# Optimization experiments

Hardware: AMD Instinct MI355X
Metric: run time of the kernel (lower is better)

## Reference

```python
import jax, jax.numpy as jnp
import numpy as np

W, L, K, N = 32, 64, 512, 64


def setup_inputs() -> dict:
    key = jax.random.key(0)
    k0, k1, k2, k3 = jax.random.split(key, 4)
    # 0/1 spin states stored as float, matching torch.randint(0, 2, ..., dtype=float32)
    states = jax.random.randint(k0, (W, L, K, N), 0, 2).astype(jnp.float32)
    Q = jax.random.normal(k1, (W, N, N), dtype=jnp.float32)
    # inverse temperatures, ascending (standard parallel-tempering ladder)
    beta = jnp.sort(jax.random.uniform(k2, (L,), minval=0.1, maxval=2.0, dtype=jnp.float32))
    # uniform draws replacing torch.rand_like(delta) in exchange()
    u = jax.random.uniform(k3, (W, L - 1, K), dtype=jnp.float32)
    return {"states": states, "Q": Q, "beta": beta, "u": u}


def reference(states, Q, beta, u):
    """Temperer.exchange(): energies then masked replica swap.

    Returns (energies (W,L,K) before exchange, new states (W,L,K,N)).
    """
    # energy: einsum('wlki,wij,wlkj->wlk') done as one GEMM + elementwise reduce
    sQ = jnp.einsum('wlki,wij->wlkj', states, Q)          # (W,L,K,N)
    energies = jnp.einsum('wlkj,wlkj->wlk', sQ, states)   # (W,L,K)

    dbeta = (beta[1:] - beta[:-1])[None, :, None]          # (1,L-1,1)
    delta = (energies[:, 1:] - energies[:, :-1]) * dbeta   # (W,L-1,K)
    mask = (u < jnp.exp(delta)).astype(states.dtype)[..., None]  # (W,L-1,K,1)

    left = states[:, :-1]
    right = states[:, 1:]
    # replicate torch's sequential overlapping slice assignments exactly
    new = states.at[:, :-1].set(mask * right + (1.0 - mask) * left)
    new = new.at[:, 1:].set(mask * left + (1.0 - mask) * right)
    return energies, new
```

## Files before the change

### kernel.cpp

```cpp
#include <hip/hip_runtime.h>
#include <math.h>

#define PW 32
#define PL 64
#define PK 512
#define PN 64

typedef int   v4i __attribute__((ext_vector_type(4)));
typedef float v4f __attribute__((ext_vector_type(4)));


constexpr int ITERS_PER_WAVE = 4;

__global__ __launch_bounds__(256) void energies_kernel(
    const float* __restrict__ states, const float* __restrict__ Q,
    float* __restrict__ e_out, double* __restrict__ e64,
    unsigned long long* __restrict__ pmask)
{
    __shared__ alignas(16) signed char Afrag[16 * 64 * 16];

    const int tid  = threadIdx.x;
    const int lane = tid & 63;
    const int wv   = tid >> 6;
    const int w    = blockIdx.x >> 6;
    const int blk  = blockIdx.x & 63;

    const float* Qw = Q + w * PN * PN;
    for (int e = tid; e < PN * PN; e += 256) {
        const int i = e >> 6, j = e & 63;
        long long R = llrint((double)Qw[e] * 268435456.0);
        const int h = i & 3, b = i >> 2;
        const int frag_lane = (h << 4) | (j & 15);
        const int jt = j >> 4;
#pragma unroll
        for (int k = 0; k < 4; ++k) {
            const signed char d = (signed char)(R & 0xFF);
            R = (R - d) >> 8;
            Afrag[((k * 4 + jt) * 64 + frag_lane) * 16 + b] = d;
        }
    }
    __syncthreads();

    const v4i* Af = (const v4i*)Afrag;

    const long vw_base = (long)w * (PL * PK)
                       + (long)(blk * 4 + wv) * (32 * ITERS_PER_WAVE);
    const int h   = lane >> 4;
    const int g16 = (lane & 3) * 16;
    const int itA = (lane & 15) >> 2;
    const int itO = (lane & 31) >> 2;

    for (int t = 0; t < ITERS_PER_WAVE; ++t) {
        const long vbase = vw_base + (long)t * 32;

        unsigned long long pmA = 0, pmB = 0, pmO = 0;
#pragma unroll
        for (int it = 0; it < 8; ++it) {
            const v4f f = ((const v4f*)(states + (vbase + it * 4) * PN))[lane];
            const unsigned long long m0 = __ballot(f.x != 0.0f);
            const unsigned long long m1 = __ballot(f.y != 0.0f);
            const unsigned long long m2 = __ballot(f.z != 0.0f);
            const unsigned long long m3 = __ballot(f.w != 0.0f);
            const unsigned long long cand =
                  ((m0 >> g16) & 0xFFFFull)
                | (((m1 >> g16) & 0xFFFFull) << 16)
                | (((m2 >> g16) & 0xFFFFull) << 32)
                | (((m3 >> g16) & 0xFFFFull) << 48);
            pmA = (it == itA)     ? cand : pmA;
            pmB = (it == itA + 4) ? cand : pmB;
            pmO = (it == itO)     ? cand : pmO;
        }
        if (lane < 32) pmask[vbase + lane] = pmO;

        const unsigned int bA = (unsigned int)(pmA >> (h * 16)) & 0xFFFFu;
        const unsigned int bB = (unsigned int)(pmB >> (h * 16)) & 0xFFFFu;
        v4i BA, BB;
#pragma unroll
        for (int q = 0; q < 4; ++q) {
            BA[q] = (int)((((bA >> (4 * q)) & 0xFu) * 0x00204081u) & 0x01010101u);
            BB[q] = (int)((((bB >> (4 * q)) & 0xFu) * 0x00204081u) & 0x01010101u);
        }

        unsigned int xA[4], xB[4];
#pragma unroll
        for (int r = 0; r < 4; ++r) {
            xA[r] = (unsigned int)(pmA >> (r * 16 + h)) & 0x1111u;
            xB[r] = (unsigned int)(pmB >> (r * 16 + h)) & 0x1111u;
        }

        long long accA = 0, accB = 0;
#pragma unroll
        for (int k = 0; k < 4; ++k) {
            v4i A0 = Af[(k * 4 + 0) * 64 + lane];
            v4i A1 = Af[(k * 4 + 1) * 64 + lane];
            v4i A2 = Af[(k * 4 + 2) * 64 + lane];
            v4i A3 = Af[(k * 4 + 3) * 64 + lane];
            v4i CA0 = {0,0,0,0}, CA1 = {0,0,0,0}, CA2 = {0,0,0,0}, CA3 = {0,0,0,0};
            v4i CB0 = {0,0,0,0}, CB1 = {0,0,0,0}, CB2 = {0,0,0,0}, CB3 = {0,0,0,0};
            asm("s_nop 1\n\t"
                "v_mfma_i32_16x16x64_i8 %0, %8, %12, %0\n\t"
                "v_mfma_i32_16x16x64_i8 %4, %8, %13, %4\n\t"
                "v_mfma_i32_16x16x64_i8 %1, %9, %12, %1\n\t"
                "v_mfma_i32_16x16x64_i8 %5, %9, %13, %5\n\t"
                "v_mfma_i32_16x16x64_i8 %2, %10, %12, %2\n\t"
                "v_mfma_i32_16x16x64_i8 %6, %10, %13, %6\n\t"
                "v_mfma_i32_16x16x64_i8 %3, %11, %12, %3\n\t"
                "v_mfma_i32_16x16x64_i8 %7, %11, %13, %7\n\t"
                "s_nop 7\n\t"
                "s_nop 7"
                : "+v"(CA0), "+v"(CA1), "+v"(CA2), "+v"(CA3),
                  "+v"(CB0), "+v"(CB1), "+v"(CB2), "+v"(CB3)
                : "v"(A0), "v"(A1), "v"(A2), "v"(A3), "v"(BA), "v"(BB));
            int akA = 0, akB = 0;
#pragma unroll
            for (int r = 0; r < 4; ++r) {
                akA += ((xA[r] >> 0)  & 1) * CA0[r];
                akA += ((xA[r] >> 4)  & 1) * CA1[r];
                akA += ((xA[r] >> 8)  & 1) * CA2[r];
                akA += ((xA[r] >> 12) & 1) * CA3[r];
                akB += ((xB[r] >> 0)  & 1) * CB0[r];
                akB += ((xB[r] >> 4)  & 1) * CB1[r];
                akB += ((xB[r] >> 8)  & 1) * CB2[r];
                akB += ((xB[r] >> 12) & 1) * CB3[r];
            }
            accA += (long long)akA << (8 * k);
            accB += (long long)akB << (8 * k);
        }

        accA += __shfl_xor(accA, 16, 64);
        accA += __shfl_xor(accA, 32, 64);
        accB += __shfl_xor(accB, 16, 64);
        accB += __shfl_xor(accB, 32, 64);

        if (lane < 16) {
            const double eA = (double)accA * 0x1p-28;
            const double eB = (double)accB * 0x1p-28;
            e64[vbase + lane]        = eA;
            e_out[vbase + lane]      = (float)eA;
            e64[vbase + 16 + lane]   = eB;
            e_out[vbase + 16 + lane] = (float)eB;
        }
    }
}

__global__ __launch_bounds__(256) void swap_kernel(
    const unsigned long long* __restrict__ pmask,
    const double* __restrict__ e64,
    const float* __restrict__ beta, const float* __restrict__ u,
    float* __restrict__ out)
{
    const long row0 = (long)blockIdx.x * 16;
    const int tid = threadIdx.x;
    const long row = row0 + (tid >> 4);
    const int e = tid & 15;
    const int w = (int)(row >> 15);
    const int l = (int)((row >> 9) & 63);
    const int k = (int)(row & 511);

    long src;
    if (l == 0) {
        const double db = (double)beta[1] - (double)beta[0];
        const double delta = (e64[row + PK] - e64[row]) * db;
        const float uv = u[(long)w * (PL - 1) * PK + k];
        src = row + (((double)uv < exp(delta)) ? PK : 0);
    } else {
        const double db = (double)beta[l] - (double)beta[l - 1];
        const double delta = (e64[row] - e64[row - PK]) * db;
        const float uv = u[((long)w * (PL - 1) + (l - 1)) * PK + k];
        src = row - (((double)uv < exp(delta)) ? PK : 0);
    }

    const unsigned long long pm = pmask[src];
    v4f f;
    f.x = ((pm >> e)        & 1) ? 1.0f : 0.0f;
    f.y = ((pm >> (16 + e)) & 1) ? 1.0f : 0.0f;
    f.z = ((pm >> (32 + e)) & 1) ? 1.0f : 0.0f;
    f.w = ((pm >> (48 + e)) & 1) ? 1.0f : 0.0f;
    ((v4f*)(out + row * PN))[e] = f;
}

extern "C" void kernel_launch(void* const* d_in, const int* in_sizes, int n_in,
                              void* d_out, int out_size, void* d_ws, size_t ws_size,
                              hipStream_t stream) {
    const float* states = (const float*)d_in[0];
    const float* Q      = (const float*)d_in[1];
    const float* beta   = (const float*)d_in[2];
    const float* u      = (const float*)d_in[3];

    float* e_out      = (float*)d_out;
    float* new_states = (float*)d_out + (long)PW * PL * PK;

    const long NV = (long)PW * PL * PK;
    double* e64 = (double*)d_ws;
    unsigned long long* pmask = (unsigned long long*)((char*)d_ws + 8 * NV);

    energies_kernel<<<2048, 256, 0, stream>>>(states, Q, e_out, e64, pmask);

    swap_kernel<<<65536, 256, 0, stream>>>(pmask, e64, beta, u, new_states);
}
```

Measured before the change: 513.5 us.

## Hoist Q fragments to registers, batch state loads, restructure swap kernel per-row decisions

Energies kernel now processes twice as many rows per wave with half the blocks, hoists all 16 Q fragments from LDS into registers once, and issues all eight state loads up front before the ballot packing to increase memory-level parallelism. Swap kernel computes one accept decision per row per thread (instead of 16 redundant threads per row), stages source offsets in shared memory, then writes 256 rows per block. This removes redundant exp/e64 loads in the swap and LDS reloads in the energy pass, at the cost of higher register pressure and fewer blocks.

```diff
diff --git a/kernel.cpp b/kernel.cpp
--- a/kernel.cpp
+++ b/kernel.cpp
@@ -10,9 +10,11 @@
 typedef float v4f __attribute__((ext_vector_type(4)));
 
 
-constexpr int ITERS_PER_WAVE = 4;
-
-__global__ __launch_bounds__(256) void energies_kernel(
+constexpr int ITERS_PER_WAVE = 8;
+
+#define DECLA(n) v4i A##n = Af[(n) * 64 + lane];
+
+__global__ __launch_bounds__(256, 3) void energies_kernel(
     const float* __restrict__ states, const float* __restrict__ Q,
     float* __restrict__ e_out, double* __restrict__ e64,
     unsigned long long* __restrict__ pmask)
@@ -22,8 +24,8 @@
     const int tid  = threadIdx.x;
     const int lane = tid & 63;
     const int wv   = tid >> 6;
-    const int w    = blockIdx.x >> 6;
-    const int blk  = blockIdx.x & 63;
+    const int w    = blockIdx.x >> 5;
+    const int blk  = blockIdx.x & 31;
 
     const float* Qw = Q + w * PN * PN;
     for (int e = tid; e < PN * PN; e += 256) {
@@ -43,6 +45,11 @@
 
     const v4i* Af = (const v4i*)Afrag;
 
+    DECLA(0)  DECLA(1)  DECLA(2)  DECLA(3)
+    DECLA(4)  DECLA(5)  DECLA(6)  DECLA(7)
+    DECLA(8)  DECLA(9)  DECLA(10) DECLA(11)
+    DECLA(12) DECLA(13) DECLA(14) DECLA(15)
+
     const long vw_base = (long)w * (PL * PK)
                        + (long)(blk * 4 + wv) * (32 * ITERS_PER_WAVE);
     const int h   = lane >> 4;
@@ -52,24 +59,36 @@
 
     for (int t = 0; t < ITERS_PER_WAVE; ++t) {
         const long vbase = vw_base + (long)t * 32;
+        const float* sp = states + vbase * PN;
+
+        v4f f0 = ((const v4f*)(sp          ))[lane];
+        v4f f1 = ((const v4f*)(sp +  4 * PN))[lane];
+        v4f f2 = ((const v4f*)(sp +  8 * PN))[lane];
+        v4f f3 = ((const v4f*)(sp + 12 * PN))[lane];
+        v4f f4 = ((const v4f*)(sp + 16 * PN))[lane];
+        v4f f5 = ((const v4f*)(sp + 20 * PN))[lane];
+        v4f f6 = ((const v4f*)(sp + 24 * PN))[lane];
+        v4f f7 = ((const v4f*)(sp + 28 * PN))[lane];
 
         unsigned long long pmA = 0, pmB = 0, pmO = 0;
-#pragma unroll
-        for (int it = 0; it < 8; ++it) {
-            const v4f f = ((const v4f*)(states + (vbase + it * 4) * PN))[lane];
-            const unsigned long long m0 = __ballot(f.x != 0.0f);
-            const unsigned long long m1 = __ballot(f.y != 0.0f);
-            const unsigned long long m2 = __ballot(f.z != 0.0f);
-            const unsigned long long m3 = __ballot(f.w != 0.0f);
-            const unsigned long long cand =
-                  ((m0 >> g16) & 0xFFFFull)
-                | (((m1 >> g16) & 0xFFFFull) << 16)
-                | (((m2 >> g16) & 0xFFFFull) << 32)
-                | (((m3 >> g16) & 0xFFFFull) << 48);
-            pmA = (it == itA)     ? cand : pmA;
-            pmB = (it == itA + 4) ? cand : pmB;
-            pmO = (it == itO)     ? cand : pmO;
-        }
+#define PACK_IT(it, ff)                                                    \
+        {                                                                  \
+            const unsigned long long m0 = __ballot(ff.x != 0.0f);          \
+            const unsigned long long m1 = __ballot(ff.y != 0.0f);          \
+            const unsigned long long m2 = __ballot(ff.z != 0.0f);          \
+            const unsigned long long m3 = __ballot(ff.w != 0.0f);          \
+            const unsigned long long cand =                                \
+                  ((m0 >> g16) & 0xFFFFull)                                \
+                | (((m1 >> g16) & 0xFFFFull) << 16)                        \
+                | (((m2 >> g16) & 0xFFFFull) << 32)                        \
+                | (((m3 >> g16) & 0xFFFFull) << 48);                       \
+            pmA = ((it) == itA)     ? cand : pmA;                          \
+            pmB = ((it) == itA + 4) ? cand : pmB;                          \
+            pmO = ((it) == itO)     ? cand : pmO;                          \
+        }
+        PACK_IT(0, f0) PACK_IT(1, f1) PACK_IT(2, f2) PACK_IT(3, f3)
+        PACK_IT(4, f4) PACK_IT(5, f5) PACK_IT(6, f6) PACK_IT(7, f7)
+#undef PACK_IT
         if (lane < 32) pmask[vbase + lane] = pmO;
 
         const unsigned int bA = (unsigned int)(pmA >> (h * 16)) & 0xFFFFu;
@@ -89,43 +108,44 @@
         }
 
         long long accA = 0, accB = 0;
-#pragma unroll
-        for (int k = 0; k < 4; ++k) {
-            v4i A0 = Af[(k * 4 + 0) * 64 + lane];
-            v4i A1 = Af[(k * 4 + 1) * 64 + lane];
-            v4i A2 = Af[(k * 4 + 2) * 64 + lane];
-            v4i A3 = Af[(k * 4 + 3) * 64 + lane];
-            v4i CA0 = {0,0,0,0}, CA1 = {0,0,0,0}, CA2 = {0,0,0,0}, CA3 = {0,0,0,0};
-            v4i CB0 = {0,0,0,0}, CB1 = {0,0,0,0}, CB2 = {0,0,0,0}, CB3 = {0,0,0,0};
-            asm("s_nop 1\n\t"
-                "v_mfma_i32_16x16x64_i8 %0, %8, %12, %0\n\t"
-                "v_mfma_i32_16x16x64_i8 %4, %8, %13, %4\n\t"
-                "v_mfma_i32_16x16x64_i8 %1, %9, %12, %1\n\t"
-                "v_mfma_i32_16x16x64_i8 %5, %9, %13, %5\n\t"
-                "v_mfma_i32_16x16x64_i8 %2, %10, %12, %2\n\t"
-                "v_mfma_i32_16x16x64_i8 %6, %10, %13, %6\n\t"
-                "v_mfma_i32_16x16x64_i8 %3, %11, %12, %3\n\t"
-                "v_mfma_i32_16x16x64_i8 %7, %11, %13, %7\n\t"
-                "s_nop 7\n\t"
-                "s_nop 7"
-                : "+v"(CA0), "+v"(CA1), "+v"(CA2), "+v"(CA3),
-                  "+v"(CB0), "+v"(CB1), "+v"(CB2), "+v"(CB3)
-                : "v"(A0), "v"(A1), "v"(A2), "v"(A3), "v"(BA), "v"(BB));
-            int akA = 0, akB = 0;
-#pragma unroll
-            for (int r = 0; r < 4; ++r) {
-                akA += ((xA[r] >> 0)  & 1) * CA0[r];
-                akA += ((xA[r] >> 4)  & 1) * CA1[r];
-                akA += ((xA[r] >> 8)  & 1) * CA2[r];
-                akA += ((xA[r] >> 12) & 1) * CA3[r];
-                akB += ((xB[r] >> 0)  & 1) * CB0[r];
-                akB += ((xB[r] >> 4)  & 1) * CB1[r];
-                akB += ((xB[r] >> 8)  & 1) * CB2[r];
-                akB += ((xB[r] >> 12) & 1) * CB3[r];
-            }
-            accA += (long long)akA << (8 * k);
-            accB += (long long)akB << (8 * k);
-        }
+#define DIGIT_K(k, a0, a1, a2, a3)                                          \
+        {                                                                   \
+            v4i CA0 = {0,0,0,0}, CA1 = {0,0,0,0}, CA2 = {0,0,0,0}, CA3 = {0,0,0,0}; \
+            v4i CB0 = {0,0,0,0}, CB1 = {0,0,0,0}, CB2 = {0,0,0,0}, CB3 = {0,0,0,0}; \
+            asm("s_nop 1\n\t"                                               \
+                "v_mfma_i32_16x16x64_i8 %0, %8, %12, %0\n\t"                \
+                "v_mfma_i32_16x16x64_i8 %4, %8, %13, %4\n\t"                \
+                "v_mfma_i32_16x16x64_i8 %1, %9, %12, %1\n\t"                \
+                "v_mfma_i32_16x16x64_i8 %5, %9, %13, %5\n\t"                \
+                "v_mfma_i32_16x16x64_i8 %2, %10, %12, %2\n\t"               \
+                "v_mfma_i32_16x16x64_i8 %6, %10, %13, %6\n\t"               \
+                "v_mfma_i32_16x16x64_i8 %3, %11, %12, %3\n\t"               \
+                "v_mfma_i32_16x16x64_i8 %7, %11, %13, %7\n\t"               \
+                "s_nop 7\n\t"                                               \
+                "s_nop 7"                                                   \
+                : "+v"(CA0), "+v"(CA1), "+v"(CA2), "+v"(CA3),               \
+                  "+v"(CB0), "+v"(CB1), "+v"(CB2), "+v"(CB3)                \
+                : "v"(a0), "v"(a1), "v"(a2), "v"(a3), "v"(BA), "v"(BB));    \
+            int akA = 0, akB = 0;                                           \
+            _Pragma("unroll")                                               \
+            for (int r = 0; r < 4; ++r) {                                   \
+                akA += ((xA[r] >> 0)  & 1) * CA0[r];                        \
+                akA += ((xA[r] >> 4)  & 1) * CA1[r];                        \
+                akA += ((xA[r] >> 8)  & 1) * CA2[r];                        \
+                akA += ((xA[r] >> 12) & 1) * CA3[r];                        \
+                akB += ((xB[r] >> 0)  & 1) * CB0[r];                        \
+                akB += ((xB[r] >> 4)  & 1) * CB1[r];                        \
+                akB += ((xB[r] >> 8)  & 1) * CB2[r];                        \
+                akB += ((xB[r] >> 12) & 1) * CB3[r];                        \
+            }                                                               \
+            accA += (long long)akA << (8 * (k));                            \
+            accB += (long long)akB << (8 * (k));                            \
+        }
+        DIGIT_K(0, A0,  A1,  A2,  A3)
+        DIGIT_K(1, A4,  A5,  A6,  A7)
+        DIGIT_K(2, A8,  A9,  A10, A11)
+        DIGIT_K(3, A12, A13, A14, A15)
+#undef DIGIT_K
 
         accA += __shfl_xor(accA, 16, 64);
         accA += __shfl_xor(accA, 32, 64);
@@ -149,34 +169,43 @@
     const float* __restrict__ beta, const float* __restrict__ u,
     float* __restrict__ out)
 {
-    const long row0 = (long)blockIdx.x * 16;
+    __shared__ int srcl[256];
     const int tid = threadIdx.x;
-    const long row = row0 + (tid >> 4);
+    const long row0 = (long)blockIdx.x * 256;
+
+    {
+        const long row = row0 + tid;
+        const int w = (int)(row >> 15);
+        const int l = (int)((row >> 9) & 63);
+        const int k = (int)(row & 511);
+        long src;
+        if (l == 0) {
+            const double db = (double)beta[1] - (double)beta[0];
+            const double delta = (e64[row + PK] - e64[row]) * db;
+            const float uv = u[(long)w * (PL - 1) * PK + k];
+            src = row + (((double)uv < exp(delta)) ? PK : 0);
+        } else {
+            const double db = (double)beta[l] - (double)beta[l - 1];
+            const double delta = (e64[row] - e64[row - PK]) * db;
+            const float uv = u[((long)w * (PL - 1) + (l - 1)) * PK + k];
+            src = row - (((double)uv < exp(delta)) ? PK : 0);
+        }
+        srcl[tid] = (int)(src - row0);
+    }
+    __syncthreads();
+
     const int e = tid & 15;
-    const int w = (int)(row >> 15);
-    const int l = (int)((row >> 9) & 63);
-    const int k = (int)(row & 511);
-
-    long src;
-    if (l == 0) {
-        const double db = (double)beta[1] - (double)beta[0];
-        const double delta = (e64[row + PK] - e64[row]) * db;
-        const float uv = u[(long)w * (PL - 1) * PK + k];
-        src = row + (((double)uv < exp(delta)) ? PK : 0);
-    } else {
-        const double db = (double)beta[l] - (double)beta[l - 1];
-        const double delta = (e64[row] - e64[row - PK]) * db;
-        const float uv = u[((long)w * (PL - 1) + (l - 1)) * PK + k];
-        src = row - (((double)uv < exp(delta)) ? PK : 0);
-    }
-
-    const unsigned long long pm = pmask[src];
-    v4f f;
-    f.x = ((pm >> e)        & 1) ? 1.0f : 0.0f;
-    f.y = ((pm >> (16 + e)) & 1) ? 1.0f : 0.0f;
-    f.z = ((pm >> (32 + e)) & 1) ? 1.0f : 0.0f;
-    f.w = ((pm >> (48 + e)) & 1) ? 1.0f : 0.0f;
-    ((v4f*)(out + row * PN))[e] = f;
+#pragma unroll
+    for (int g = 0; g < 16; ++g) {
+        const int r = g * 16 + (tid >> 4);
+        const unsigned long long pm = pmask[row0 + srcl[r]];
+        v4f f;
+        f.x = ((pm >> e)        & 1) ? 1.0f : 0.0f;
+        f.y = ((pm >> (16 + e)) & 1) ? 1.0f : 0.0f;
+        f.z = ((pm >> (32 + e)) & 1) ? 1.0f : 0.0f;
+        f.w = ((pm >> (48 + e)) & 1) ? 1.0f : 0.0f;
+        ((v4f*)(out + (row0 + r) * PN))[e] = f;
+    }
 }
 
 extern "C" void kernel_launch(void* const* d_in, const int* in_sizes, int n_in,
@@ -194,7 +223,7 @@
     double* e64 = (double*)d_ws;
     unsigned long long* pmask = (unsigned long long*)((char*)d_ws + 8 * NV);
 
-    energies_kernel<<<2048, 256, 0, stream>>>(states, Q, e_out, e64, pmask);
-
-    swap_kernel<<<65536, 256, 0, stream>>>(pmask, e64, beta, u, new_states);
+    energies_kernel<<<1024, 256, 0, stream>>>(states, Q, e_out, e64, pmask);
+
+    swap_kernel<<<4096, 256, 0, stream>>>(pmask, e64, beta, u, new_states);
 }
```

New measurement: 493.9 us. 1.04x faster.
